# Kernel optimization log

Measured on AMD Instinct MI355X. Metric: run time of the kernel, lower is better.

The kernel has to match this reference:

```python
import jax, jax.numpy as jnp
import numpy as np

B, S, D = 1, 2048, 2048
H, KVH = 32, 8
HD = D // H          # 64
N_REP = H // KVH     # 4
ROPE_THETA = 10000.0
NEG = -1e9


def setup_inputs() -> dict:
    key = jax.random.key(0)
    ks = jax.random.split(key, 8)
    x = jax.random.normal(ks[0], (B, S, D), dtype=jnp.float32)
    # RoPE tables: freqs_cis[t, j] = exp(i * t * theta^{-2j/HD}), j in [0, HD/2)
    inv_freq = 1.0 / (ROPE_THETA ** (jnp.arange(0, HD, 2, dtype=jnp.float32) / HD))
    angles = jnp.arange(S, dtype=jnp.float32)[:, None] * inv_freq[None, :]  # (S, HD/2)
    freqs_cos = jnp.cos(angles)
    freqs_sin = jnp.sin(angles)
    # causal additive mask (S, S)
    mask = jnp.where(jnp.tril(jnp.ones((S, S), dtype=bool)), 0.0, NEG).astype(jnp.float32)
    sc = 0.02
    wq = jax.random.normal(ks[1], (D, H * HD), dtype=jnp.float32) * sc
    wk = jax.random.normal(ks[2], (D, KVH * HD), dtype=jnp.float32) * sc
    wv = jax.random.normal(ks[3], (D, KVH * HD), dtype=jnp.float32) * sc
    wo = jax.random.normal(ks[4], (H * HD, D), dtype=jnp.float32) * sc
    fw = jax.random.normal(ks[5], (HD, HD), dtype=jnp.float32) * sc
    fb = jnp.zeros((HD,), dtype=jnp.float32)
    return {"x": x, "freqs_cos": freqs_cos, "freqs_sin": freqs_sin, "mask": mask,
            "wq": wq, "wk": wk, "wv": wv, "wo": wo, "fw": fw, "fb": fb,
            "start_pos": 0}


def _rope(t, cos, sin):
    # t: (B, S, h, HD) -> complex rotate pairs along last dim
    tr = t.reshape(*t.shape[:-1], HD // 2, 2)
    c = cos[None, :, None, :]  # (1, S, 1, HD/2)
    s = sin[None, :, None, :]
    re = tr[..., 0] * c - tr[..., 1] * s
    im = tr[..., 0] * s + tr[..., 1] * c
    return jnp.stack([re, im], axis=-1).reshape(t.shape)


def reference(x, freqs_cos, freqs_sin, mask, wq, wk, wv, wo, fw, fb, start_pos):
    b, s, _ = x.shape
    xq = (x @ wq).reshape(b, s, H, HD)
    xk = (x @ wk).reshape(b, s, KVH, HD)
    xv = (x @ wv).reshape(b, s, KVH, HD)
    xq = _rope(xq, freqs_cos, freqs_sin)
    xk = _rope(xk, freqs_cos, freqs_sin)
    # GQA: repeat kv heads (repeat_interleave on head dim)
    keys = jnp.repeat(xk, N_REP, axis=2)    # (b, s, H, HD)
    values = jnp.repeat(xv, N_REP, axis=2)
    q = xq.transpose(0, 2, 1, 3)            # (b, H, s, HD)
    k = keys.transpose(0, 2, 1, 3)
    v = values.transpose(0, 2, 1, 3)
    scores = jnp.einsum("bhqd,bhkd->bhqk", q, k) / np.sqrt(HD).astype(np.float32)
    scores = scores + mask[None, None, :, :]
    probs = jax.nn.softmax(scores.astype(jnp.float32), axis=-1).astype(q.dtype)
    out = jnp.einsum("bhqk,bhkd->bhqd", probs, v)  # (b, H, s, HD)
    # shared per-head FFN: Linear(HD, HD) + SiLU, vectorized over heads
    out = jax.nn.silu(out @ fw + fb)
    out = out.transpose(0, 2, 1, 3).reshape(b, s, H * HD)
    return out @ wo
```

## Files before the change

kernel.cpp:

```cpp
#include <hip/hip_runtime.h>
#include <stdint.h>

#define S_LEN 2048
#define DMODEL 2048
#define NH 32
#define NKV 8
#define HD 64

typedef __attribute__((ext_vector_type(8))) __bf16 bf16x8;
typedef __attribute__((ext_vector_type(4))) float f32x4;
typedef __attribute__((ext_vector_type(16))) float f32x16;

__device__ __forceinline__ unsigned short f2bf(float f) {
    union { float f; uint32_t u; } v; v.f = f;
    uint32_t u = v.u;
    u += 0x7FFFu + ((u >> 16) & 1u);
    return (unsigned short)(u >> 16);
}

__device__ __forceinline__ float bf2f(unsigned short b) {
    union { uint32_t u; float f; } v;
    v.u = ((uint32_t)b) << 16;
    return v.f;
}

__device__ __forceinline__ uint32_t cvt_pk_bf16(float lo, float hi) {
    uint32_t r;
    asm("v_cvt_pk_bf16_f32 %0, %1, %2" : "=v"(r) : "v"(lo), "v"(hi));
    return r;
}

#define GLDS16(g, l)                                                          \
    __builtin_amdgcn_global_load_lds(                                         \
        (const __attribute__((address_space(1))) unsigned int*)(g),           \
        (__attribute__((address_space(3))) unsigned int*)(l), 16, 0, 0)

__device__ const int kUQT[24] = {15,15,7,14,14,13,13,6,12,12,11,11,5,10,10,9,9,4,8,8,3,2,1,0};
__device__ const int kUCH[24] = {0,1,0,0,1,0,1,0,0,1,0,1,0,0,1,0,1,0,0,1,0,0,0,0};
__device__ const int kUSP[24] = {1,1,0,1,1,1,1,0,1,1,1,1,0,1,1,1,1,0,1,1,0,0,0,0};

__global__ void cast_bf16_kernel(const float* __restrict__ src,
                                 unsigned short* __restrict__ dst, int n) {
    int g = (blockIdx.x * blockDim.x + threadIdx.x) * 8;
    if (g >= n) return;
    float4 a = *(const float4*)&src[g];
    float4 b = *(const float4*)&src[g + 4];
    unsigned short o[8];
    o[0] = f2bf(a.x); o[1] = f2bf(a.y); o[2] = f2bf(a.z); o[3] = f2bf(a.w);
    o[4] = f2bf(b.x); o[5] = f2bf(b.y); o[6] = f2bf(b.z); o[7] = f2bf(b.w);
    *(uint4*)&dst[g] = *(const uint4*)o;
}

__global__ void transpose_cast_kernel(const float* __restrict__ src,
                                      unsigned short* __restrict__ dst,
                                      int R, int C) {
    __shared__ float tile[32][33];
    int c0 = blockIdx.x * 32, r0 = blockIdx.y * 32;
    int tx = threadIdx.x, ty = threadIdx.y;
#pragma unroll
    for (int i = 0; i < 32; i += 8)
        tile[ty + i][tx] = src[(size_t)(r0 + ty + i) * C + c0 + tx];
    __syncthreads();
#pragma unroll
    for (int i = 0; i < 32; i += 8)
        dst[(size_t)(c0 + ty + i) * R + r0 + tx] = f2bf(tile[tx][ty + i]);
}

template <bool BF16OUT>
__global__ __launch_bounds__(256) void gemm_bt_kernel(
    const unsigned short* __restrict__ A, const unsigned short* __restrict__ BT,
    float* __restrict__ C0, float* __restrict__ C1,
    unsigned short* __restrict__ Cb, int M, int N, int Kstride, int Klen) {
    __shared__ unsigned short As[3][128 * 32];
    __shared__ unsigned short Bs[3][128 * 32];
    const int t = threadIdx.x;
    const int lane = t & 63, wave = t >> 6;
    const int wr = wave >> 1, wc = wave & 1;
    const int gx = gridDim.x;
    const int nwg = gx * gridDim.y;
    const int wg = blockIdx.y * gx + blockIdx.x;
    const int swz = (wg & 7) * (nwg >> 3) + (wg >> 3);
    const int m0 = (swz % gx) * 128, n0 = (swz / gx) * 128;
    const int koff = blockIdx.z * Klen;
    const int l15 = lane & 15, lhi = lane >> 4;
    f32x4 acc[4][4] = {};
    const unsigned short* ga = A + (size_t)(m0 + (t >> 2)) * Kstride + koff + (t & 3) * 8;
    const unsigned short* gb = BT + (size_t)(n0 + (t >> 2)) * Kstride + koff + (t & 3) * 8;
    const int nk = Klen >> 5;

#define GSTAGE(buf, kt)                                                       \
    {                                                                         \
        const int k0_ = (kt) * 32;                                            \
        GLDS16(ga + k0_, &As[buf][t * 8]);                                    \
        GLDS16(ga + (size_t)64 * Kstride + k0_, &As[buf][t * 8 + 64 * 32]);   \
        GLDS16(gb + k0_, &Bs[buf][t * 8]);                                    \
        GLDS16(gb + (size_t)64 * Kstride + k0_, &Bs[buf][t * 8 + 64 * 32]);   \
    }

    GSTAGE(0, 0);
    GSTAGE(1, 1);

    int cb = 0, pfb = 2;
#pragma unroll 1
    for (int kt = 0; kt < nk; ++kt) {
        if (kt + 1 < nk) asm volatile("s_waitcnt vmcnt(4)" ::: "memory");
        else             asm volatile("s_waitcnt vmcnt(0)" ::: "memory");
        __builtin_amdgcn_s_barrier();
        __builtin_amdgcn_sched_barrier(0);
        if (kt + 2 < nk) GSTAGE(pfb, kt + 2);
        pfb = (pfb == 2) ? 0 : pfb + 1;
        const int mycb = cb;
        cb = (cb == 2) ? 0 : cb + 1;
        bf16x8 af[4], bfr[4];
#pragma unroll
        for (int m = 0; m < 4; m++)
            af[m] = *(const bf16x8*)&As[mycb][(wr * 64 + m * 16 + l15) * 32 + lhi * 8];
#pragma unroll
        for (int n = 0; n < 4; n++)
            bfr[n] = *(const bf16x8*)&Bs[mycb][(wc * 64 + n * 16 + l15) * 32 + lhi * 8];
#pragma unroll
        for (int m = 0; m < 4; m++)
#pragma unroll
            for (int n = 0; n < 4; n++)
                acc[m][n] = __builtin_amdgcn_mfma_f32_16x16x32_bf16(
                    af[m], bfr[n], acc[m][n], 0, 0, 0);
    }
#undef GSTAGE
#pragma unroll
    for (int m = 0; m < 4; m++) {
        int row = m0 + wr * 64 + m * 16 + lhi * 4;
#pragma unroll
        for (int n = 0; n < 4; n++) {
            int col = n0 + wc * 64 + n * 16 + l15;
            if (BF16OUT) {
#pragma unroll
                for (int r = 0; r < 4; r++)
                    Cb[(size_t)(row + r) * N + col] = f2bf(acc[m][n][r]);
            } else {
                float* __restrict__ C = blockIdx.z ? C1 : C0;
#pragma unroll
                for (int r = 0; r < 4; r++)
                    C[(size_t)(row + r) * N + col] = acc[m][n][r];
            }
        }
    }
}

__global__ void add_f32_kernel(float* __restrict__ out,
                               const float* __restrict__ p1, int n4) {
    int g = blockIdx.x * blockDim.x + threadIdx.x;
    if (g >= n4) return;
    float4 a = *(const float4*)&out[g * 4];
    float4 b = *(const float4*)&p1[g * 4];
    a.x += b.x; a.y += b.y; a.z += b.z; a.w += b.w;
    *(float4*)&out[g * 4] = a;
}

__global__ void rope_q_kernel(const unsigned short* __restrict__ Cqkv,
                              const float* __restrict__ cb,
                              const float* __restrict__ sb,
                              unsigned short* __restrict__ Q) {
    const float CS = 0.125f * 1.44269504f;
    int g = blockIdx.x * 256 + threadIdx.x;
    int i = g & 31;
    int h = (g >> 5) & 31;
    int s = g >> 10;
    ushort2 v = *(const ushort2*)&Cqkv[(size_t)s * 3072 + h * 64 + 2 * i];
    float vx = bf2f(v.x), vy = bf2f(v.y);
    float cc = cb[s * 32 + i], ss = sb[s * 32 + i];
    ushort2 o;
    o.x = f2bf((vx * cc - vy * ss) * CS);
    o.y = f2bf((vx * ss + vy * cc) * CS);
    *(ushort2*)&Q[(size_t)h * (S_LEN * HD) + s * HD + 2 * i] = o;
}

__global__ void rope_k_kernel(const unsigned short* __restrict__ Cqkv,
                              const float* __restrict__ cb,
                              const float* __restrict__ sb,
                              unsigned short* __restrict__ Kb) {
    int g = blockIdx.x * 256 + threadIdx.x;
    int i = g & 31;
    int kvh = (g >> 5) & 7;
    int s = g >> 8;
    ushort2 v = *(const ushort2*)&Cqkv[(size_t)s * 3072 + 2048 + kvh * 64 + 2 * i];
    float vx = bf2f(v.x), vy = bf2f(v.y);
    float cc = cb[s * 32 + i], ss = sb[s * 32 + i];
    ushort2 o;
    o.x = f2bf(vx * cc - vy * ss);
    o.y = f2bf(vx * ss + vy * cc);
    *(ushort2*)&Kb[(size_t)kvh * (S_LEN * HD) + s * HD + 2 * i] = o;
}

__global__ void v_transpose_kernel(const unsigned short* __restrict__ Cqkv,
                                   unsigned short* __restrict__ VT) {
    __shared__ unsigned short tile[32][33];
    int kvh = blockIdx.z;
    int d0 = blockIdx.x * 32, s0 = blockIdx.y * 32;
    int tx = threadIdx.x, ty = threadIdx.y;
#pragma unroll
    for (int i = 0; i < 32; i += 8)
        tile[ty + i][tx] =
            Cqkv[(size_t)(s0 + ty + i) * 3072 + 2560 + kvh * 64 + d0 + tx];
    __syncthreads();
#pragma unroll
    for (int i = 0; i < 32; i += 8)
        VT[(size_t)kvh * (HD * S_LEN) + (size_t)(d0 + ty + i) * S_LEN + s0 + tx] =
            tile[tx][ty + i];
}

__global__ __launch_bounds__(256) void flash_kernel(
    const unsigned short* __restrict__ Q, const unsigned short* __restrict__ Kg,
    const unsigned short* __restrict__ VTg, unsigned short* __restrict__ O,
    float* __restrict__ Opart, float* __restrict__ ML) {
    __shared__ unsigned short Ks[3][4096];
    __shared__ unsigned short Vs[3][4096];
    const int t = threadIdx.x, lane = t & 63, wave = t >> 6;
    const int l31 = lane & 31, hi = lane >> 5;
    const int bid = blockIdx.x;
    const int h = bid & 31, u = bid >> 5;
    const int qt = kUQT[u], ch = kUCH[u], sp = kUSP[u];
    const int kvh = h >> 2;

    const int kt0 = sp ? ch * (qt + 1) : 0;
    const int ktN = sp ? kt0 + qt + 1 : 2 * qt + 2;

    const int srow = t >> 3;
    const int scol = ((t & 7) * 8) ^ ((srow & 7) * 8);
    const unsigned short* gk = Kg + ((size_t)kvh * S_LEN + srow) * HD + scol;
    const unsigned short* gv = VTg + ((size_t)kvh * HD + srow) * S_LEN + scol;

    const int q0 = qt * 128;
    const int qw0 = q0 + wave * 32;
    const int q = qw0 + l31;

    const unsigned short* qp = Q + ((size_t)h * S_LEN + q) * HD + hi * 8;
    bf16x8 qf0 = *(const bf16x8*)(qp);
    bf16x8 qf1 = *(const bf16x8*)(qp + 16);
    bf16x8 qf2 = *(const bf16x8*)(qp + 32);
    bf16x8 qf3 = *(const bf16x8*)(qp + 48);

    f32x16 oacc0 = {}, oacc1 = {};
    float mrun = -1e30f, lrun = 0.f;

    {
        const size_t kva = (size_t)kt0 * 64, kvb = kva + 64;
        GLDS16(gk + kva * HD, &Ks[0][t * 8]);
        GLDS16(gk + (kva + 32) * HD, &Ks[0][t * 8 + 2048]);
        GLDS16(gv + kva, &Vs[0][t * 8]);
        GLDS16(gv + (size_t)32 * S_LEN + kva, &Vs[0][t * 8 + 2048]);
        GLDS16(gk + kvb * HD, &Ks[1][t * 8]);
        GLDS16(gk + (kvb + 32) * HD, &Ks[1][t * 8 + 2048]);
        GLDS16(gv + kvb, &Vs[1][t * 8]);
        GLDS16(gv + (size_t)32 * S_LEN + kvb, &Vs[1][t * 8 + 2048]);
    }

    int cb = 0, pfb = 2;
#pragma unroll 1
    for (int kt = kt0; kt < ktN; ++kt) {
        if (kt + 1 < ktN) asm volatile("s_waitcnt vmcnt(4)" ::: "memory");
        else              asm volatile("s_waitcnt vmcnt(0)" ::: "memory");
        __builtin_amdgcn_s_barrier();
        __builtin_amdgcn_sched_barrier(0);
        if (kt + 2 < ktN) {
            const size_t kvp = (size_t)(kt + 2) * 64;
            GLDS16(gk + kvp * HD, &Ks[pfb][t * 8]);
            GLDS16(gk + (kvp + 32) * HD, &Ks[pfb][t * 8 + 2048]);
            GLDS16(gv + kvp, &Vs[pfb][t * 8]);
            GLDS16(gv + (size_t)32 * S_LEN + kvp, &Vs[pfb][t * 8 + 2048]);
        }
        pfb = (pfb == 2) ? 0 : pfb + 1;
        const int kv0 = kt * 64;
        const int mycb = cb;
        cb = (cb == 2) ? 0 : cb + 1;
        if (kv0 > qw0 + 31) continue;
        const unsigned short* ksb = Ks[mycb];
        const unsigned short* vsb = Vs[mycb];
        const int sw = (l31 & 7) * 8;
        f32x16 s0 = {}, s1 = {};
#pragma unroll
        for (int kc = 0; kc < 4; kc++) {
            bf16x8 k0 = *(const bf16x8*)&ksb[l31 * 64 + ((16 * kc + 8 * hi) ^ sw)];
            bf16x8 k1 = *(const bf16x8*)&ksb[(32 + l31) * 64 + ((16 * kc + 8 * hi) ^ sw)];
            bf16x8 qc = (kc == 0) ? qf0 : (kc == 1) ? qf1 : (kc == 2) ? qf2 : qf3;
            s0 = __builtin_amdgcn_mfma_f32_32x32x16_bf16(k0, qc, s0, 0, 0, 0);
            s1 = __builtin_amdgcn_mfma_f32_32x32x16_bf16(k1, qc, s1, 0, 0, 0);
        }
        float p0[16], p1[16];
        if (kv0 + 63 <= qw0) {
#pragma unroll
            for (int r = 0; r < 16; r++) { p0[r] = s0[r]; p1[r] = s1[r]; }
        } else {
#pragma unroll
            for (int r = 0; r < 16; r++) {
                int rr = (r & 3) + 8 * (r >> 2) + 4 * hi;
                p0[r] = (kv0 + rr <= q) ? s0[r] : -1e30f;
                p1[r] = (kv0 + 32 + rr <= q) ? s1[r] : -1e30f;
            }
        }
        float t8[8];
#pragma unroll
        for (int r = 0; r < 8; r++)
            t8[r] = fmaxf(fmaxf(p0[r], p0[r + 8]), fmaxf(p1[r], p1[r + 8]));
        float lm = fmaxf(fmaxf(fmaxf(t8[0], t8[4]), fmaxf(t8[1], t8[5])),
                         fmaxf(fmaxf(t8[2], t8[6]), fmaxf(t8[3], t8[7])));
        if (!__all(lm - mrun <= 8.f)) {
            float rm = fmaxf(lm, __shfl_xor(lm, 32));
            float mnew = fmaxf(mrun, rm);
            float sc = exp2f(mrun - mnew);
            mrun = mnew;
            lrun *= sc;
            oacc0 *= sc;
            oacc1 *= sc;
        }
#pragma unroll
        for (int r = 0; r < 16; r++) {
            p0[r] = exp2f(p0[r] - mrun);
            p1[r] = exp2f(p1[r] - mrun);
        }
        float sA = 0.f, sB = 0.f, sC = 0.f, sD = 0.f;
#pragma unroll
        for (int r = 0; r < 4; r++) {
            sA += p0[r] + p1[r];
            sB += p0[r + 4] + p1[r + 4];
            sC += p0[r + 8] + p1[r + 8];
            sD += p0[r + 12] + p1[r + 12];
        }
        lrun += (sA + sB) + (sC + sD);
        bf16x8 pf[4];
#pragma unroll
        for (int kc = 0; kc < 4; kc++) {
            const int sub = (kc & 1) * 8;
            uint32_t Wl0, Wl1, Wh0, Wh1;
            if (kc < 2) {
                Wl0 = cvt_pk_bf16(p0[sub + 0], p0[sub + 1]);
                Wl1 = cvt_pk_bf16(p0[sub + 2], p0[sub + 3]);
                Wh0 = cvt_pk_bf16(p0[sub + 4], p0[sub + 5]);
                Wh1 = cvt_pk_bf16(p0[sub + 6], p0[sub + 7]);
            } else {
                Wl0 = cvt_pk_bf16(p1[sub + 0], p1[sub + 1]);
                Wl1 = cvt_pk_bf16(p1[sub + 2], p1[sub + 3]);
                Wh0 = cvt_pk_bf16(p1[sub + 4], p1[sub + 5]);
                Wh1 = cvt_pk_bf16(p1[sub + 6], p1[sub + 7]);
            }
            uint32_t sw0 = hi ? Wl0 : Wh0, sw1 = hi ? Wl1 : Wh1;
            uint32_t rc0 = __shfl_xor((int)sw0, 32);
            uint32_t rc1 = __shfl_xor((int)sw1, 32);
            uint32_t kp0 = hi ? Wh0 : Wl0, kp1 = hi ? Wh1 : Wl1;
            uint32_t F0 = hi ? rc0 : kp0;
            uint32_t F1 = hi ? rc1 : kp1;
            uint32_t F2 = hi ? kp0 : rc0;
            uint32_t F3 = hi ? kp1 : rc1;
            uint4 fu = {F0, F1, F2, F3};
            pf[kc] = *(const bf16x8*)&fu;
        }
#pragma unroll
        for (int kc = 0; kc < 4; kc++) {
            bf16x8 v0 = *(const bf16x8*)&vsb[l31 * 64 + ((16 * kc + 8 * hi) ^ sw)];
            bf16x8 v1 = *(const bf16x8*)&vsb[(32 + l31) * 64 + ((16 * kc + 8 * hi) ^ sw)];
            oacc0 = __builtin_amdgcn_mfma_f32_32x32x16_bf16(v0, pf[kc], oacc0, 0, 0, 0);
            oacc1 = __builtin_amdgcn_mfma_f32_32x32x16_bf16(v1, pf[kc], oacc1, 0, 0, 0);
        }
    }
    lrun += __shfl_xor(lrun, 32);
    const int qrow = wave * 32 + l31;
    if (sp) {
        const int pidx = (h * 8 + (qt - 8)) * 2 + ch;
        float* po = Opart + ((size_t)pidx * 128 + qrow) * 64 + 4 * hi;
#pragma unroll
        for (int g = 0; g < 4; g++) {
            float4 a = {oacc0[4 * g], oacc0[4 * g + 1], oacc0[4 * g + 2], oacc0[4 * g + 3]};
            *(float4*)(po + 8 * g) = a;
            float4 b = {oacc1[4 * g], oacc1[4 * g + 1], oacc1[4 * g + 2], oacc1[4 * g + 3]};
            *(float4*)(po + 32 + 8 * g) = b;
        }
        if (hi == 0) {
            ML[((size_t)pidx * 128 + qrow) * 2] = mrun;
            ML[((size_t)pidx * 128 + qrow) * 2 + 1] = lrun;
        }
    } else {
        float rinv = 1.f / lrun;
        unsigned short* ob = O + ((size_t)h * S_LEN + q) * HD + 4 * hi;
#pragma unroll
        for (int g = 0; g < 4; g++) {
            uint32_t a0 = cvt_pk_bf16(oacc0[4 * g] * rinv, oacc0[4 * g + 1] * rinv);
            uint32_t a1 = cvt_pk_bf16(oacc0[4 * g + 2] * rinv, oacc0[4 * g + 3] * rinv);
            uint2 u0 = {a0, a1};
            *(uint2*)(ob + 8 * g) = u0;
            uint32_t b0 = cvt_pk_bf16(oacc1[4 * g] * rinv, oacc1[4 * g + 1] * rinv);
            uint32_t b1 = cvt_pk_bf16(oacc1[4 * g + 2] * rinv, oacc1[4 * g + 3] * rinv);
            uint2 u1 = {b0, b1};
            *(uint2*)(ob + 32 + 8 * g) = u1;
        }
    }
}

__global__ __launch_bounds__(256) void flash_combine_kernel(
    const float* __restrict__ Opart, const float* __restrict__ ML,
    unsigned short* __restrict__ attn) {
    const int bid = blockIdx.x;
    const int h = bid & 31, j = bid >> 5;
    const int qt = 8 + j;
    const int t = threadIdx.x;
    const int qrow = t >> 1, d0 = (t & 1) * 32;
    const int base = (h * 8 + j) * 2;
    const float mA = ML[((size_t)base * 128 + qrow) * 2];
    const float lA = ML[((size_t)base * 128 + qrow) * 2 + 1];
    const float mB = ML[((size_t)(base + 1) * 128 + qrow) * 2];
    const float lB = ML[((size_t)(base + 1) * 128 + qrow) * 2 + 1];
    const float m = fmaxf(mA, mB);
    const float wA = exp2f(mA - m), wB = exp2f(mB - m);
    const float rinv = 1.f / (lA * wA + lB * wB);
    const float* pA = Opart + ((size_t)base * 128 + qrow) * 64 + d0;
    const float* pB = Opart + ((size_t)(base + 1) * 128 + qrow) * 64 + d0;
    unsigned short* po = attn + ((size_t)h * S_LEN + qt * 128 + qrow) * HD + d0;
#pragma unroll
    for (int dd = 0; dd < 32; dd += 8) {
        float4 a0 = *(const float4*)&pA[dd], a1 = *(const float4*)&pA[dd + 4];
        float4 b0 = *(const float4*)&pB[dd], b1 = *(const float4*)&pB[dd + 4];
        unsigned short o[8];
        o[0] = f2bf((a0.x * wA + b0.x * wB) * rinv);
        o[1] = f2bf((a0.y * wA + b0.y * wB) * rinv);
        o[2] = f2bf((a0.z * wA + b0.z * wB) * rinv);
        o[3] = f2bf((a0.w * wA + b0.w * wB) * rinv);
        o[4] = f2bf((a1.x * wA + b1.x * wB) * rinv);
        o[5] = f2bf((a1.y * wA + b1.y * wB) * rinv);
        o[6] = f2bf((a1.z * wA + b1.z * wB) * rinv);
        o[7] = f2bf((a1.w * wA + b1.w * wB) * rinv);
        *(uint4*)&po[dd] = *(const uint4*)o;
    }
}

__global__ __launch_bounds__(256) void fw_silu_kernel(
    const unsigned short* __restrict__ AT, const unsigned short* __restrict__ fwT,
    const float* __restrict__ fb, unsigned short* __restrict__ h2) {
    const int t = threadIdx.x, lane = t & 63, wave = t >> 6;
    const int l15 = lane & 15, lhi = lane >> 4;
    const int r0 = blockIdx.x * 64 + wave * 16;
    const unsigned short* ap = AT + (size_t)(r0 + l15) * HD + lhi * 8;
    bf16x8 a0 = *(const bf16x8*)ap;
    bf16x8 a1 = *(const bf16x8*)(ap + 32);
    f32x4 acc[4] = {};
#pragma unroll
    for (int nb = 0; nb < 4; nb++) {
        const unsigned short* bp = fwT + (size_t)(nb * 16 + l15) * HD + lhi * 8;
        bf16x8 b0 = *(const bf16x8*)bp;
        bf16x8 b1 = *(const bf16x8*)(bp + 32);
        acc[nb] = __builtin_amdgcn_mfma_f32_16x16x32_bf16(a0, b0, acc[nb], 0, 0, 0);
        acc[nb] = __builtin_amdgcn_mfma_f32_16x16x32_bf16(a1, b1, acc[nb], 0, 0, 0);
    }
#pragma unroll
    for (int nb = 0; nb < 4; nb++) {
        int col = nb * 16 + l15;
        float bias = fb[col];
#pragma unroll
        for (int r = 0; r < 4; r++) {
            int row = r0 + lhi * 4 + r;
            int s = row & (S_LEN - 1), hh = row >> 11;
            float x = acc[nb][r] + bias;
            float sg = 1.f / (1.f + exp2f(-x * 1.44269504f));
            h2[(size_t)s * DMODEL + hh * HD + col] = f2bf(x * sg);
        }
    }
}

extern "C" void kernel_launch(void* const* d_in, const int* in_sizes, int n_in,
                              void* d_out, int out_size, void* d_ws, size_t ws_size,
                              hipStream_t stream) {
    const float* x = (const float*)d_in[0];
    const float* fcos = (const float*)d_in[1];
    const float* fsin = (const float*)d_in[2];
    const float* wq = (const float*)d_in[4];
    const float* wk = (const float*)d_in[5];
    const float* wv = (const float*)d_in[6];
    const float* wo = (const float*)d_in[7];
    const float* fw = (const float*)d_in[8];
    const float* fb = (const float*)d_in[9];
    float* out = (float*)d_out;

    char* ws = (char*)d_ws;
    size_t off = 0;
    auto alloc = [&](size_t bytes) {
        void* p = ws + off;
        off += (bytes + 255) & ~(size_t)255;
        return p;
    };
    unsigned short* wqkvT = (unsigned short*)alloc((size_t)3072 * 2048 * 2);
    unsigned short* woT   = (unsigned short*)alloc((size_t)2048 * 2048 * 2);
    unsigned short* fwT   = (unsigned short*)alloc((size_t)64 * 64 * 2);
    unsigned short* Cqkv  = (unsigned short*)alloc((size_t)2048 * 3072 * 2);
    unsigned short* Qb    = (unsigned short*)alloc((size_t)NH * S_LEN * HD * 2);
    unsigned short* Kb    = (unsigned short*)alloc((size_t)NKV * S_LEN * HD * 2);
    unsigned short* VT    = (unsigned short*)alloc((size_t)NKV * HD * S_LEN * 2);
    unsigned short* xb    = (unsigned short*)alloc((size_t)2048 * 2048 * 2);
    float*          ML    = (float*)alloc((size_t)512 * 128 * 2 * 4);
    unsigned short* attn  = (unsigned short*)alloc((size_t)NH * S_LEN * HD * 2);
    float*          P1    = (float*)alloc((size_t)2048 * 2048 * 4);
    float* Opart = P1;
    unsigned short* h2 = xb;

    dim3 tb(32, 8);
    cast_bf16_kernel<<<2048, 256, 0, stream>>>(x, xb, 2048 * 2048);
    transpose_cast_kernel<<<dim3(64, 64), tb, 0, stream>>>(wq, wqkvT, 2048, 2048);
    transpose_cast_kernel<<<dim3(16, 64), tb, 0, stream>>>(wk, wqkvT + (size_t)2048 * 2048, 2048, 512);
    transpose_cast_kernel<<<dim3(16, 64), tb, 0, stream>>>(wv, wqkvT + (size_t)2560 * 2048, 2048, 512);
    transpose_cast_kernel<<<dim3(64, 64), tb, 0, stream>>>(wo, woT, 2048, 2048);
    transpose_cast_kernel<<<dim3(2, 2), tb, 0, stream>>>(fw, fwT, 64, 64);

    gemm_bt_kernel<true><<<dim3(16, 24, 1), 256, 0, stream>>>(
        xb, wqkvT, nullptr, nullptr, Cqkv, 2048, 3072, 2048, 2048);

    rope_q_kernel<<<8192, 256, 0, stream>>>(Cqkv, fcos, fsin, Qb);
    rope_k_kernel<<<2048, 256, 0, stream>>>(Cqkv, fcos, fsin, Kb);
    v_transpose_kernel<<<dim3(2, 64, 8), tb, 0, stream>>>(Cqkv, VT);

    flash_kernel<<<768, 256, 0, stream>>>(Qb, Kb, VT, attn, Opart, ML);
    flash_combine_kernel<<<256, 256, 0, stream>>>(Opart, ML, attn);

    fw_silu_kernel<<<1024, 256, 0, stream>>>(attn, fwT, fb, h2);

    gemm_bt_kernel<false><<<dim3(16, 16, 2), 256, 0, stream>>>(
        h2, woT, out, P1, nullptr, 2048, 2048, 2048, 1024);
    add_f32_kernel<<<4096, 256, 0, stream>>>(out, P1, 1048576);
}
```

Baseline: 189.4 us.

## Use 128x64 GEMM tiles and drop split-K with its add kernel

The GEMM tile changes from 128x128 to 128x64, so the QKV projection launches 768 workgroups instead of 384 and the output projection launches 512. The output projection's split-K over two partials, along with its separate add kernel and fp32 partial buffer, is removed. The goal is enough workgroups to fill the CUs without the extra partial-sum traffic and launch. Smaller tiles lower MFMA reuse per byte loaded and raise redundant A-tile loads.

```diff
diff --git a/kernel.cpp b/kernel.cpp
--- a/kernel.cpp
+++ b/kernel.cpp
@@ -69,10 +69,10 @@
 template <bool BF16OUT>
 __global__ __launch_bounds__(256) void gemm_bt_kernel(
     const unsigned short* __restrict__ A, const unsigned short* __restrict__ BT,
-    float* __restrict__ C0, float* __restrict__ C1,
-    unsigned short* __restrict__ Cb, int M, int N, int Kstride, int Klen) {
+    float* __restrict__ C0, unsigned short* __restrict__ Cb,
+    int M, int N, int K) {
     __shared__ unsigned short As[3][128 * 32];
-    __shared__ unsigned short Bs[3][128 * 32];
+    __shared__ unsigned short Bs[3][64 * 32];
     const int t = threadIdx.x;
     const int lane = t & 63, wave = t >> 6;
     const int wr = wave >> 1, wc = wave & 1;
@@ -80,21 +80,19 @@
     const int nwg = gx * gridDim.y;
     const int wg = blockIdx.y * gx + blockIdx.x;
     const int swz = (wg & 7) * (nwg >> 3) + (wg >> 3);
-    const int m0 = (swz % gx) * 128, n0 = (swz / gx) * 128;
-    const int koff = blockIdx.z * Klen;
+    const int m0 = (swz % gx) * 128, n0 = (swz / gx) * 64;
     const int l15 = lane & 15, lhi = lane >> 4;
-    f32x4 acc[4][4] = {};
-    const unsigned short* ga = A + (size_t)(m0 + (t >> 2)) * Kstride + koff + (t & 3) * 8;
-    const unsigned short* gb = BT + (size_t)(n0 + (t >> 2)) * Kstride + koff + (t & 3) * 8;
-    const int nk = Klen >> 5;
+    f32x4 acc[4][2] = {};
+    const unsigned short* ga = A + (size_t)(m0 + (t >> 2)) * K + (t & 3) * 8;
+    const unsigned short* gb = BT + (size_t)(n0 + (t >> 2)) * K + (t & 3) * 8;
+    const int nk = K >> 5;
 
 #define GSTAGE(buf, kt)                                                       \
     {                                                                         \
         const int k0_ = (kt) * 32;                                            \
         GLDS16(ga + k0_, &As[buf][t * 8]);                                    \
-        GLDS16(ga + (size_t)64 * Kstride + k0_, &As[buf][t * 8 + 64 * 32]);   \
-        GLDS16(gb + k0_, &Bs[buf][t * 8]);                                    \
-        GLDS16(gb + (size_t)64 * Kstride + k0_, &Bs[buf][t * 8 + 64 * 32]);   \
+        GLDS16(ga + (size_t)64 * K + k0_, &As[buf][t * 8 + 64 * 32]);         \
+        if (t < 256) GLDS16(gb + k0_, &Bs[buf][t * 8]);                       \
     }
 
     GSTAGE(0, 0);
@@ -103,7 +101,7 @@
     int cb = 0, pfb = 2;
 #pragma unroll 1
     for (int kt = 0; kt < nk; ++kt) {
-        if (kt + 1 < nk) asm volatile("s_waitcnt vmcnt(4)" ::: "memory");
+        if (kt + 1 < nk) asm volatile("s_waitcnt vmcnt(3)" ::: "memory");
         else             asm volatile("s_waitcnt vmcnt(0)" ::: "memory");
         __builtin_amdgcn_s_barrier();
         __builtin_amdgcn_sched_barrier(0);
@@ -111,17 +109,17 @@
         pfb = (pfb == 2) ? 0 : pfb + 1;
         const int mycb = cb;
         cb = (cb == 2) ? 0 : cb + 1;
-        bf16x8 af[4], bfr[4];
+        bf16x8 af[4], bfr[2];
 #pragma unroll
         for (int m = 0; m < 4; m++)
             af[m] = *(const bf16x8*)&As[mycb][(wr * 64 + m * 16 + l15) * 32 + lhi * 8];
 #pragma unroll
-        for (int n = 0; n < 4; n++)
-            bfr[n] = *(const bf16x8*)&Bs[mycb][(wc * 64 + n * 16 + l15) * 32 + lhi * 8];
+        for (int n = 0; n < 2; n++)
+            bfr[n] = *(const bf16x8*)&Bs[mycb][(wc * 32 + n * 16 + l15) * 32 + lhi * 8];
 #pragma unroll
         for (int m = 0; m < 4; m++)
 #pragma unroll
-            for (int n = 0; n < 4; n++)
+            for (int n = 0; n < 2; n++)
                 acc[m][n] = __builtin_amdgcn_mfma_f32_16x16x32_bf16(
                     af[m], bfr[n], acc[m][n], 0, 0, 0);
     }
@@ -130,30 +128,19 @@
     for (int m = 0; m < 4; m++) {
         int row = m0 + wr * 64 + m * 16 + lhi * 4;
 #pragma unroll
-        for (int n = 0; n < 4; n++) {
-            int col = n0 + wc * 64 + n * 16 + l15;
+        for (int n = 0; n < 2; n++) {
+            int col = n0 + wc * 32 + n * 16 + l15;
             if (BF16OUT) {
 #pragma unroll
                 for (int r = 0; r < 4; r++)
                     Cb[(size_t)(row + r) * N + col] = f2bf(acc[m][n][r]);
             } else {
-                float* __restrict__ C = blockIdx.z ? C1 : C0;
 #pragma unroll
                 for (int r = 0; r < 4; r++)
-                    C[(size_t)(row + r) * N + col] = acc[m][n][r];
+                    C0[(size_t)(row + r) * N + col] = acc[m][n][r];
             }
         }
     }
-}
-
-__global__ void add_f32_kernel(float* __restrict__ out,
-                               const float* __restrict__ p1, int n4) {
-    int g = blockIdx.x * blockDim.x + threadIdx.x;
-    if (g >= n4) return;
-    float4 a = *(const float4*)&out[g * 4];
-    float4 b = *(const float4*)&p1[g * 4];
-    a.x += b.x; a.y += b.y; a.z += b.z; a.w += b.w;
-    *(float4*)&out[g * 4] = a;
 }
 
 __global__ void rope_q_kernel(const unsigned short* __restrict__ Cqkv,
@@ -494,8 +481,7 @@
     unsigned short* xb    = (unsigned short*)alloc((size_t)2048 * 2048 * 2);
     float*          ML    = (float*)alloc((size_t)512 * 128 * 2 * 4);
     unsigned short* attn  = (unsigned short*)alloc((size_t)NH * S_LEN * HD * 2);
-    float*          P1    = (float*)alloc((size_t)2048 * 2048 * 4);
-    float* Opart = P1;
+    float*          Opart = (float*)alloc((size_t)512 * 128 * 64 * 4);
     unsigned short* h2 = xb;
 
     dim3 tb(32, 8);
@@ -506,8 +492,8 @@
     transpose_cast_kernel<<<dim3(64, 64), tb, 0, stream>>>(wo, woT, 2048, 2048);
     transpose_cast_kernel<<<dim3(2, 2), tb, 0, stream>>>(fw, fwT, 64, 64);
 
-    gemm_bt_kernel<true><<<dim3(16, 24, 1), 256, 0, stream>>>(
-        xb, wqkvT, nullptr, nullptr, Cqkv, 2048, 3072, 2048, 2048);
+    gemm_bt_kernel<true><<<dim3(16, 48), 256, 0, stream>>>(
+        xb, wqkvT, nullptr, Cqkv, 2048, 3072, 2048);
 
     rope_q_kernel<<<8192, 256, 0, stream>>>(Cqkv, fcos, fsin, Qb);
     rope_k_kernel<<<2048, 256, 0, stream>>>(Cqkv, fcos, fsin, Kb);
@@ -518,7 +504,6 @@
 
     fw_silu_kernel<<<1024, 256, 0, stream>>>(attn, fwT, fb, h2);
 
-    gemm_bt_kernel<false><<<dim3(16, 16, 2), 256, 0, stream>>>(
-        h2, woT, out, P1, nullptr, 2048, 2048, 2048, 1024);
-    add_f32_kernel<<<4096, 256, 0, stream>>>(out, P1, 1048576);
-}
+    gemm_bt_kernel<false><<<dim3(16, 32), 256, 0, stream>>>(
+        h2, woT, out, nullptr, 2048, 2048, 2048);
+}
```

Result: faster. 183.8 us (-3.0%).
